# Performance work log

Measured on AMD Instinct MI355X. Metric: run time of the kernel, lower is better.

The kernel has to match this reference:

```python
import jax, jax.numpy as jnp
import numpy as np

H, DH = 8, 64          # num_heads, dim_heads
B, N, D = 1, 4096, 512  # batch, seq, model dim
M, CD = 256, 768        # context len, context dim
J = N + 1 + M           # kv length: self + null + context


def _ln(x, scale, bias, eps=1e-6):
    mu = x.mean(-1, keepdims=True)
    var = ((x - mu) ** 2).mean(-1, keepdims=True)
    return (x - mu) * jax.lax.rsqrt(var + eps) * scale + bias


def setup_inputs() -> dict:
    key = jax.random.key(0)
    ks = jax.random.split(key, 8)
    return {
        'x': jax.random.normal(ks[0], (B, N, D), jnp.float32),
        'context': jax.random.normal(ks[1], (B, M, CD), jnp.float32),
        'attn_bias': jax.random.normal(ks[2], (B, H, N, J), jnp.float32) * 0.02,
        'mask': jnp.ones((B, N + M), dtype=bool),
        'ln1_scale': jnp.ones((D,), jnp.float32),
        'ln1_bias': jnp.zeros((D,), jnp.float32),
        'wq': jax.random.normal(ks[3], (D, H * DH), jnp.float32) * (D ** -0.5),
        'wkv': jax.random.normal(ks[4], (D, 2 * DH), jnp.float32) * (D ** -0.5),
        'null_kv': jax.random.normal(ks[5], (2, DH), jnp.float32),
        'ln_ctx_scale': jnp.ones((CD,), jnp.float32),
        'ln_ctx_bias': jnp.zeros((CD,), jnp.float32),
        'wckv': jax.random.normal(ks[6], (CD, 2 * DH), jnp.float32) * (CD ** -0.5),
        'bckv': jnp.zeros((2 * DH,), jnp.float32),
        'wo': jax.random.normal(ks[7], (H * DH, D), jnp.float32) * ((H * DH) ** -0.5),
        'ln_out_scale': jnp.ones((D,), jnp.float32),
        'ln_out_bias': jnp.zeros((D,), jnp.float32),
    }


def reference(x, context, attn_bias, mask, ln1_scale, ln1_bias, wq, wkv,
              null_kv, ln_ctx_scale, ln_ctx_bias, wckv, bckv, wo,
              ln_out_scale, ln_out_bias):
    b, n, d = x.shape
    scale = DH ** -0.5
    xh = _ln(x, ln1_scale, ln1_bias)
    # multi-query: q has heads, k/v are shared (no head dim)
    q = (xh @ wq).reshape(b, n, H, DH).transpose(0, 2, 1, 3) * scale  # b h n d
    k, v = jnp.split(xh @ wkv, 2, axis=-1)                            # b n d each
    # null kv token appended (per source: concat (k, nk))
    nk = jnp.broadcast_to(null_kv[0], (b, 1, DH))
    nv = jnp.broadcast_to(null_kv[1], (b, 1, DH))
    k = jnp.concatenate((k, nk), axis=-2)
    v = jnp.concatenate((v, nv), axis=-2)
    # cross-attention context kv (Dense with bias)
    ch = _ln(context, ln_ctx_scale, ln_ctx_bias)
    ck, cv = jnp.split(ch @ wckv + bckv, 2, axis=-1)
    k = jnp.concatenate((k, ck), axis=-2)  # b j d, j = n+1+m
    v = jnp.concatenate((v, cv), axis=-2)
    sim = jnp.einsum('bhid,bjd->bhij', q, k) + attn_bias
    # pad mask with True for the extra (null) slot, as in source
    m = jnp.pad(mask, ((0, 0), (1, 0)), constant_values=True)[:, None, None, :]
    sim = jnp.where(m, sim, -jnp.finfo(sim.dtype).max)
    attn = jax.nn.softmax(sim, axis=-1)
    out = jnp.einsum('bhij,bjd->bhid', attn, v)
    out = out.transpose(0, 2, 1, 3).reshape(b, n, H * DH) @ wo
    return _ln(out, ln_out_scale, ln_out_bias)
```

## Files before the change

kernel.cpp:

```cpp
#include <hip/hip_runtime.h>
#include <cstdint>
#include <cstddef>

typedef unsigned short u16;
typedef short s16x8 __attribute__((ext_vector_type(8)));
typedef u16 u16x8 __attribute__((ext_vector_type(8)));
typedef u16 u16x4 __attribute__((ext_vector_type(4)));
typedef float f32x4 __attribute__((ext_vector_type(4)));

#define AS1 __attribute__((address_space(1)))
#define AS3 __attribute__((address_space(3)))

#define HH 8
#define DH 64
#define NN 4096
#define DD 512
#define MM 256
#define CDIM 768
#define JTOT 4353
#define JPAD 4416
#define NJT 69
#define SPLITJ 4
#define TILES_PER_SPLIT 18

static __device__ __forceinline__ u16 f2bf(float f) {
    unsigned int u = __builtin_bit_cast(unsigned int, f);
    u += 0x7FFFu + ((u >> 16) & 1u);
    return (u16)(u >> 16);
}
static __device__ __forceinline__ float bf2f(u16 v) {
    unsigned int u = ((unsigned int)v) << 16;
    return __builtin_bit_cast(float, u);
}

static __device__ __forceinline__ f32x4 mfma16(s16x8 a, s16x8 b, f32x4 c) {
    return __builtin_amdgcn_mfma_f32_16x16x32_bf16(a, b, c, 0, 0, 0);
}

static __device__ __forceinline__ void gload16(const void* g, void* l) {
    __builtin_amdgcn_global_load_lds((const AS1 unsigned int*)g,
                                     (AS3 unsigned int*)l, 16, 0, 0);
}

__global__ void conv_wqkv(const float* __restrict__ wq, const float* __restrict__ wkv,
                          u16* __restrict__ Wt) {
    int idx = blockIdx.x * 256 + threadIdx.x;
    int n = idx >> 9, k = idx & 511;
    float v = (n < 512) ? wq[(size_t)k * 512 + n] * 0.125f
                        : wkv[(size_t)k * 128 + (n - 512)];
    Wt[idx] = f2bf(v);
}

__global__ void conv_wckv(const float* __restrict__ w, u16* __restrict__ Wt) {
    int idx = blockIdx.x * 256 + threadIdx.x;
    int n = idx / 768, k = idx - n * 768;
    Wt[idx] = f2bf(w[(size_t)k * 128 + n]);
}

__global__ void conv_wo(const float* __restrict__ w, u16* __restrict__ Wt) {
    int idx = blockIdx.x * 256 + threadIdx.x;
    int n = idx >> 9, k = idx & 511;
    Wt[idx] = f2bf(w[(size_t)k * 512 + n]);
}

__global__ __launch_bounds__(256) void ln512_to_bf16(
    const float* __restrict__ x, const float* __restrict__ sc,
    const float* __restrict__ bi, u16* __restrict__ out) {
    int row = blockIdx.x * 4 + (threadIdx.x >> 6);
    int lane = threadIdx.x & 63;
    const float4* xp = (const float4*)(x + (size_t)row * 512);
    float4 a = xp[lane], b = xp[64 + lane];
    float s = a.x + a.y + a.z + a.w + b.x + b.y + b.z + b.w;
    float q = a.x*a.x + a.y*a.y + a.z*a.z + a.w*a.w
            + b.x*b.x + b.y*b.y + b.z*b.z + b.w*b.w;
    #pragma unroll
    for (int m = 1; m < 64; m <<= 1) { s += __shfl_xor(s, m); q += __shfl_xor(q, m); }
    float mu = s * (1.f / 512.f);
    float var = q * (1.f / 512.f) - mu * mu;
    float rs = rsqrtf(var + 1e-6f);
    const float4* sp = (const float4*)sc;
    const float4* bp = (const float4*)bi;
    float4 s0 = sp[lane], s1 = sp[64 + lane], b0 = bp[lane], b1 = bp[64 + lane];
    u16x4 o0, o1;
    o0[0] = f2bf((a.x - mu) * rs * s0.x + b0.x);
    o0[1] = f2bf((a.y - mu) * rs * s0.y + b0.y);
    o0[2] = f2bf((a.z - mu) * rs * s0.z + b0.z);
    o0[3] = f2bf((a.w - mu) * rs * s0.w + b0.w);
    o1[0] = f2bf((b.x - mu) * rs * s1.x + b1.x);
    o1[1] = f2bf((b.y - mu) * rs * s1.y + b1.y);
    o1[2] = f2bf((b.z - mu) * rs * s1.z + b1.z);
    o1[3] = f2bf((b.w - mu) * rs * s1.w + b1.w);
    u16x4* op = (u16x4*)(out + (size_t)row * 512);
    op[lane] = o0;
    op[64 + lane] = o1;
}

__global__ __launch_bounds__(256) void ln768_to_bf16(
    const float* __restrict__ x, const float* __restrict__ sc,
    const float* __restrict__ bi, u16* __restrict__ out) {
    int row = blockIdx.x * 4 + (threadIdx.x >> 6);
    int lane = threadIdx.x & 63;
    const float4* xp = (const float4*)(x + (size_t)row * 768);
    float4 a = xp[lane], b = xp[64 + lane], c = xp[128 + lane];
    float s = a.x+a.y+a.z+a.w + b.x+b.y+b.z+b.w + c.x+c.y+c.z+c.w;
    float q = a.x*a.x+a.y*a.y+a.z*a.z+a.w*a.w + b.x*b.x+b.y*b.y+b.z*b.z+b.w*b.w
            + c.x*c.x+c.y*c.y+c.z*c.z+c.w*c.w;
    #pragma unroll
    for (int m = 1; m < 64; m <<= 1) { s += __shfl_xor(s, m); q += __shfl_xor(q, m); }
    float mu = s * (1.f / 768.f);
    float var = q * (1.f / 768.f) - mu * mu;
    float rs = rsqrtf(var + 1e-6f);
    const float4* sp = (const float4*)sc;
    const float4* bp = (const float4*)bi;
    u16x4* op = (u16x4*)(out + (size_t)row * 768);
    #pragma unroll
    for (int seg = 0; seg < 3; ++seg) {
        float4 v = (seg == 0) ? a : (seg == 1) ? b : c;
        float4 ss = sp[seg * 64 + lane], bb = bp[seg * 64 + lane];
        u16x4 o;
        o[0] = f2bf((v.x - mu) * rs * ss.x + bb.x);
        o[1] = f2bf((v.y - mu) * rs * ss.y + bb.y);
        o[2] = f2bf((v.z - mu) * rs * ss.z + bb.z);
        o[3] = f2bf((v.w - mu) * rs * ss.w + bb.w);
        op[seg * 64 + lane] = o;
    }
}

__global__ __launch_bounds__(256) void ln512_to_f32(
    const float* __restrict__ x, const float* __restrict__ sc,
    const float* __restrict__ bi, float* __restrict__ out) {
    int row = blockIdx.x * 4 + (threadIdx.x >> 6);
    int lane = threadIdx.x & 63;
    const float4* xp = (const float4*)(x + (size_t)row * 512);
    float4 a = xp[lane], b = xp[64 + lane];
    float s = a.x + a.y + a.z + a.w + b.x + b.y + b.z + b.w;
    float q = a.x*a.x + a.y*a.y + a.z*a.z + a.w*a.w
            + b.x*b.x + b.y*b.y + b.z*b.z + b.w*b.w;
    #pragma unroll
    for (int m = 1; m < 64; m <<= 1) { s += __shfl_xor(s, m); q += __shfl_xor(q, m); }
    float mu = s * (1.f / 512.f);
    float var = q * (1.f / 512.f) - mu * mu;
    float rs = rsqrtf(var + 1e-6f);
    const float4* sp = (const float4*)sc;
    const float4* bp = (const float4*)bi;
    float4 s0 = sp[lane], s1 = sp[64 + lane], b0 = bp[lane], b1 = bp[64 + lane];
    float4 o0, o1;
    o0.x = (a.x - mu) * rs * s0.x + b0.x;
    o0.y = (a.y - mu) * rs * s0.y + b0.y;
    o0.z = (a.z - mu) * rs * s0.z + b0.z;
    o0.w = (a.w - mu) * rs * s0.w + b0.w;
    o1.x = (b.x - mu) * rs * s1.x + b1.x;
    o1.y = (b.y - mu) * rs * s1.y + b1.y;
    o1.z = (b.z - mu) * rs * s1.z + b1.z;
    o1.w = (b.w - mu) * rs * s1.w + b1.w;
    float4* op = (float4*)(out + (size_t)row * 512);
    op[lane] = o0;
    op[64 + lane] = o1;
}

__global__ void fill_null_pad(const float* __restrict__ null_kv,
                              u16* __restrict__ Kall, u16* __restrict__ Vall) {
    int t = threadIdx.x;
    if (t < 64) {
        Kall[(size_t)4096 * 64 + t] = f2bf(null_kv[t]);
        Vall[(size_t)4096 * 64 + t] = f2bf(null_kv[64 + t]);
    }
    for (int i = t; i < (JPAD - JTOT) * 64; i += 256) {
        Kall[(size_t)JTOT * 64 + i] = 0;
        Vall[(size_t)JTOT * 64 + i] = 0;
    }
}

__global__ __launch_bounds__(256) void gemm_bf16(
    const u16* __restrict__ A, int lda, const u16* __restrict__ Bt, int ldb,
    int M, int N, int K, int mode, const float* __restrict__ bias128,
    u16* __restrict__ outQ, u16* __restrict__ outK, u16* __restrict__ outV,
    float* __restrict__ outF) {
    __shared__ __align__(16) u16 Al[128 * 32];
    __shared__ __align__(16) u16 Bl[64 * 32];
    const int tid = threadIdx.x, wave = tid >> 6, lane = tid & 63;
    const int l16 = lane & 15, l4 = lane >> 4;
    const int m0 = blockIdx.x * 128, n0 = blockIdx.y * 64;

    f32x4 acc[2][4] = {};
    const int ms = tid >> 2, ks = (tid & 3) * 8;

    for (int k0 = 0; k0 < K; k0 += 32) {
        __syncthreads();
        gload16(A + (size_t)(m0 + ms) * lda + (k0 + ks), (char*)Al + wave * 1024);
        gload16(A + (size_t)(m0 + 64 + ms) * lda + (k0 + ks), (char*)Al + 4096 + wave * 1024);
        gload16(Bt + (size_t)(n0 + ms) * ldb + (k0 + ks), (char*)Bl + wave * 1024);
        __syncthreads();
        s16x8 af[2], bf[4];
        #pragma unroll
        for (int mf = 0; mf < 2; ++mf)
            af[mf] = *(const s16x8*)&Al[(wave * 32 + mf * 16 + l16) * 32 + l4 * 8];
        #pragma unroll
        for (int nf = 0; nf < 4; ++nf)
            bf[nf] = *(const s16x8*)&Bl[(nf * 16 + l16) * 32 + l4 * 8];
        #pragma unroll
        for (int mf = 0; mf < 2; ++mf)
            #pragma unroll
            for (int nf = 0; nf < 4; ++nf)
                acc[mf][nf] = mfma16(af[mf], bf[nf], acc[mf][nf]);
    }

    #pragma unroll
    for (int mf = 0; mf < 2; ++mf)
        #pragma unroll
        for (int nf = 0; nf < 4; ++nf)
            #pragma unroll
            for (int r = 0; r < 4; ++r) {
                float v = acc[mf][nf][r];
                int m = m0 + wave * 32 + mf * 16 + l4 * 4 + r;
                int n = n0 + nf * 16 + l16;
                if (mode == 0) {
                    if (n < 512)       outQ[(size_t)m * 512 + n] = f2bf(v);
                    else if (n < 576)  outK[(size_t)m * 64 + (n - 512)] = f2bf(v);
                    else               outV[(size_t)m * 64 + (n - 576)] = f2bf(v);
                } else if (mode == 1) {
                    v += bias128[n];
                    if (n < 64) outK[(size_t)(4097 + m) * 64 + n] = f2bf(v);
                    else        outV[(size_t)(4097 + m) * 64 + (n - 64)] = f2bf(v);
                } else {
                    outF[(size_t)m * 512 + n] = v;
                }
            }
}

__global__ __launch_bounds__(256, 4) void attn_fwd(
    const u16* __restrict__ Q, const u16* __restrict__ Kall,
    const u16* __restrict__ Vall, const float* __restrict__ bias,
    u16* __restrict__ Opart, float* __restrict__ ml) {
    __shared__ __align__(16) u16 Kl[64][72];
    __shared__ __align__(16) u16 Vt[64][72];
    __shared__ __align__(16) u16 Pl[4][16][72];

    const int tid = threadIdx.x, wave = tid >> 6, lane = tid & 63;
    const int l16 = lane & 15, l4 = lane >> 4;
    const int qb = blockIdx.x, h = blockIdx.y, sp = blockIdx.z;
    const int tbeg = sp * TILES_PER_SPLIT;
    const int tend = (tbeg + TILES_PER_SPLIT < NJT) ? tbeg + TILES_PER_SPLIT : NJT;
    const int i0 = qb * 64 + wave * 16;

    const u16* qbase = Q + (size_t)(i0 + l16) * 512 + h * 64 + l4 * 8;
    s16x8 qf0 = *(const s16x8*)qbase;
    s16x8 qf1 = *(const s16x8*)(qbase + 32);

    f32x4 po[4] = {};
    float mrow[4], lrow[4];
    #pragma unroll
    for (int r = 0; r < 4; ++r) { mrow[r] = -3.0e38f; lrow[r] = 0.f; }

    const int krow = tid >> 2, kc = (tid & 3) * 16;
    const int vrow = tid & 63, vd0 = (tid >> 6) * 16;

    const float* brow = bias + ((size_t)h * NN + i0 + l4 * 4) * JTOT;

    u16x8 ks0, ks1, vs0, vs1;
    float bc[16];

#define LOAD_KV(J0) do { \
        const u16* g_ = Kall + (size_t)((J0) + krow) * 64 + kc; \
        ks0 = *(const u16x8*)g_; ks1 = *(const u16x8*)(g_ + 8); \
        const u16* gv_ = Vall + (size_t)((J0) + vrow) * 64 + vd0; \
        vs0 = *(const u16x8*)gv_; vs1 = *(const u16x8*)(gv_ + 8); \
    } while (0)

#define LOAD_BIAS(JT) do { \
        _Pragma("unroll") \
        for (int js_ = 0; js_ < 4; ++js_) { \
            int col_ = (JT) * 64 + js_ * 16 + l16; \
            bool v_ = col_ < JTOT; \
            _Pragma("unroll") \
            for (int r_ = 0; r_ < 4; ++r_) \
                bc[js_ * 4 + r_] = v_ ? brow[(size_t)r_ * JTOT + col_] : 0.f; \
        } \
    } while (0)

#define STORE_LDS() do { \
        *(u16x8*)&Kl[krow][kc]     = ks0; \
        *(u16x8*)&Kl[krow][kc + 8] = ks1; \
        _Pragma("unroll") \
        for (int e_ = 0; e_ < 8; ++e_) Vt[vd0 + e_][vrow] = vs0[e_]; \
        _Pragma("unroll") \
        for (int e_ = 0; e_ < 8; ++e_) Vt[vd0 + 8 + e_][vrow] = vs1[e_]; \
    } while (0)

    LOAD_KV(tbeg * 64);
    LOAD_BIAS(tbeg);
    STORE_LDS();
    __syncthreads();

    for (int jt = tbeg; jt < tend; ++jt) {
        const bool last = (jt == tend - 1);

        f32x4 s[4];
        #pragma unroll
        for (int js = 0; js < 4; ++js) {
            s16x8 kf0 = *(const s16x8*)&Kl[js * 16 + l16][l4 * 8];
            s16x8 kf1 = *(const s16x8*)&Kl[js * 16 + l16][32 + l4 * 8];
            f32x4 z = {};
            z = mfma16(qf0, kf0, z);
            z = mfma16(qf1, kf1, z);
            s[js] = z;
        }
        #pragma unroll
        for (int js = 0; js < 4; ++js) {
            const int col = jt * 64 + js * 16 + l16;
            const bool valid = (col < JTOT);
            #pragma unroll
            for (int r = 0; r < 4; ++r)
                s[js][r] = valid ? s[js][r] + bc[js * 4 + r] : -3.0e38f;
        }
        if (!last) {
            LOAD_BIAS(jt + 1);
            LOAD_KV((jt + 1) * 64);
        }
        float mnew[4], alpha[4];
        #pragma unroll
        for (int r = 0; r < 4; ++r) {
            float t = fmaxf(fmaxf(s[0][r], s[1][r]), fmaxf(s[2][r], s[3][r]));
            t = fmaxf(t, __shfl_xor(t, 1));
            t = fmaxf(t, __shfl_xor(t, 2));
            t = fmaxf(t, __shfl_xor(t, 4));
            t = fmaxf(t, __shfl_xor(t, 8));
            mnew[r] = fmaxf(mrow[r], t);
            alpha[r] = __expf(mrow[r] - mnew[r]);
            mrow[r] = mnew[r];
        }
        #pragma unroll
        for (int js = 0; js < 4; ++js)
            #pragma unroll
            for (int r = 0; r < 4; ++r)
                s[js][r] = __expf(s[js][r] - mnew[r]);
        #pragma unroll
        for (int r = 0; r < 4; ++r) {
            float t = s[0][r] + s[1][r] + s[2][r] + s[3][r];
            t += __shfl_xor(t, 1);
            t += __shfl_xor(t, 2);
            t += __shfl_xor(t, 4);
            t += __shfl_xor(t, 8);
            lrow[r] = lrow[r] * alpha[r] + t;
        }
        #pragma unroll
        for (int df = 0; df < 4; ++df)
            #pragma unroll
            for (int r = 0; r < 4; ++r)
                po[df][r] *= alpha[r];
        #pragma unroll
        for (int js = 0; js < 4; ++js)
            #pragma unroll
            for (int r = 0; r < 4; ++r)
                Pl[wave][l4 * 4 + r][js * 16 + l16] = f2bf(s[js][r]);
        s16x8 pa0 = *(const s16x8*)&Pl[wave][l16][l4 * 8];
        s16x8 pa1 = *(const s16x8*)&Pl[wave][l16][32 + l4 * 8];
        #pragma unroll
        for (int df = 0; df < 4; ++df) {
            s16x8 vf0 = *(const s16x8*)&Vt[df * 16 + l16][l4 * 8];
            s16x8 vf1 = *(const s16x8*)&Vt[df * 16 + l16][32 + l4 * 8];
            po[df] = mfma16(pa0, vf0, po[df]);
            po[df] = mfma16(pa1, vf1, po[df]);
        }
        if (!last) {
            __syncthreads();
            STORE_LDS();
            __syncthreads();
        }
    }

    const size_t obase = (((size_t)sp * 64 + qb) * 8 + h) * 4096;
    #pragma unroll
    for (int df = 0; df < 4; ++df)
        #pragma unroll
        for (int r = 0; r < 4; ++r)
            Opart[obase + (size_t)(wave * 16 + l4 * 4 + r) * 64 + df * 16 + l16] =
                f2bf(po[df][r]);
    const size_t mbase = (((size_t)sp * 64 + qb) * 8 + h) * 128;
    if (l16 == 0) {
        #pragma unroll
        for (int r = 0; r < 4; ++r) {
            ml[mbase + wave * 16 + l4 * 4 + r]      = mrow[r];
            ml[mbase + 64 + wave * 16 + l4 * 4 + r] = lrow[r];
        }
    }
#undef LOAD_KV
#undef LOAD_BIAS
#undef STORE_LDS
}

__global__ __launch_bounds__(256) void attn_combine(
    const u16* __restrict__ Opart, const float* __restrict__ ml,
    u16* __restrict__ Ob) {
    const int qb = blockIdx.x, h = blockIdx.y;
    const int t = threadIdx.x;
    const int row = t >> 2, d0 = (t & 3) * 16;

    float m[SPLITJ], l[SPLITJ];
    #pragma unroll
    for (int s = 0; s < SPLITJ; ++s) {
        const float* mlp = ml + (((size_t)s * 64 + qb) * 8 + h) * 128;
        m[s] = mlp[row];
        l[s] = mlp[64 + row];
    }
    float mstar = m[0];
    #pragma unroll
    for (int s = 1; s < SPLITJ; ++s) mstar = fmaxf(mstar, m[s]);

    float osum[16] = {};
    float lsum = 0.f;
    #pragma unroll
    for (int s = 0; s < SPLITJ; ++s) {
        float w = __expf(m[s] - mstar);
        lsum += w * l[s];
        const u16* op = Opart + ((((size_t)s * 64 + qb) * 8 + h) * 64 + row) * 64 + d0;
        u16x8 a = *(const u16x8*)op;
        u16x8 b = *(const u16x8*)(op + 8);
        #pragma unroll
        for (int e = 0; e < 8; ++e) {
            osum[e]     += w * bf2f(a[e]);
            osum[8 + e] += w * bf2f(b[e]);
        }
    }
    float inv = 1.f / lsum;
    u16x8 oa, obv;
    #pragma unroll
    for (int e = 0; e < 8; ++e) {
        oa[e]  = f2bf(osum[e] * inv);
        obv[e] = f2bf(osum[8 + e] * inv);
    }
    u16* dst = Ob + (size_t)(qb * 64 + row) * 512 + h * 64 + d0;
    *(u16x8*)dst = oa;
    *(u16x8*)(dst + 8) = obv;
}

extern "C" void kernel_launch(void* const* d_in, const int* in_sizes, int n_in,
                              void* d_out, int out_size, void* d_ws, size_t ws_size,
                              hipStream_t stream) {
    (void)in_sizes; (void)n_in; (void)out_size; (void)ws_size;
    const float* x     = (const float*)d_in[0];
    const float* ctx   = (const float*)d_in[1];
    const float* bias  = (const float*)d_in[2];
    const float* ln1s  = (const float*)d_in[4];
    const float* ln1b  = (const float*)d_in[5];
    const float* wq    = (const float*)d_in[6];
    const float* wkv   = (const float*)d_in[7];
    const float* nullkv= (const float*)d_in[8];
    const float* lncs  = (const float*)d_in[9];
    const float* lncb  = (const float*)d_in[10];
    const float* wckv  = (const float*)d_in[11];
    const float* bckv  = (const float*)d_in[12];
    const float* wo    = (const float*)d_in[13];
    const float* lnos  = (const float*)d_in[14];
    const float* lnob  = (const float*)d_in[15];
    float* out = (float*)d_out;

    char* ws = (char*)d_ws;
    u16*   Wo_   = (u16*)(ws + 0);
    u16*   Wqkv  = (u16*)(ws + 524288);
    float* Ml    = (float*)(ws + 524288);
    u16*   Wckv  = (u16*)(ws + 1179648);
    u16*   ch    = (u16*)(ws + 1572864);
    u16*   Qb    = (u16*)(ws + 1966080);
    u16*   Ob    = (u16*)(ws + 1966080);
    u16*   Kall  = (u16*)(ws + 6160384);
    u16*   Vall  = (u16*)(ws + 6725632);
    u16*   xh    = (u16*)(ws + 7290880);
    u16*   Opart = (u16*)(ws + 7290880);
    float* tmp   = (float*)(ws + 7290880);

    conv_wqkv<<<(640 * 512) / 256, 256, 0, stream>>>(wq, wkv, Wqkv);
    conv_wckv<<<(128 * 768) / 256, 256, 0, stream>>>(wckv, Wckv);
    conv_wo<<<(512 * 512) / 256, 256, 0, stream>>>(wo, Wo_);
    ln512_to_bf16<<<1024, 256, 0, stream>>>(x, ln1s, ln1b, xh);
    ln768_to_bf16<<<64, 256, 0, stream>>>(ctx, lncs, lncb, ch);
    fill_null_pad<<<1, 256, 0, stream>>>(nullkv, Kall, Vall);
    gemm_bf16<<<dim3(32, 10), 256, 0, stream>>>(xh, 512, Wqkv, 512, 4096, 640, 512,
                                                0, nullptr, Qb, Kall, Vall, nullptr);
    gemm_bf16<<<dim3(2, 2), 256, 0, stream>>>(ch, 768, Wckv, 768, 256, 128, 768,
                                              1, bckv, nullptr, Kall, Vall, nullptr);
    attn_fwd<<<dim3(64, 8, SPLITJ), 256, 0, stream>>>(Qb, Kall, Vall, bias, Opart, Ml);
    attn_combine<<<dim3(64, 8), 256, 0, stream>>>(Opart, Ml, Ob);
    gemm_bf16<<<dim3(32, 8), 256, 0, stream>>>(Ob, 512, Wo_, 512, 4096, 512, 512,
                                               2, nullptr, nullptr, nullptr, nullptr, tmp);
    ln512_to_f32<<<1024, 256, 0, stream>>>(tmp, lnos, lnob, out);
}
```

Measured before the change: 277.7 us.

## Store V transposed in global memory and read K/V fragments directly, dropping LDS staging

The GEMM epilogues now write V in a transposed [d][JPAD] layout, and the null and pad fill is adjusted to match. The attention kernel loads K and V MFMA fragments straight from global memory (through cache) instead of staging them in LDS with a scattered transpose. This removes two block-wide barriers per tile and the LDS transpose stores. In exchange, each wave issues its own redundant global loads, with no register prefetch ahead of use, so it relies on L1/L2 hits to hide latency. The transposed V stores in the GEMM epilogue are also strided.

```diff
diff --git a/kernel.cpp b/kernel.cpp
--- a/kernel.cpp
+++ b/kernel.cpp
@@ -159,15 +159,16 @@
 }
 
 __global__ void fill_null_pad(const float* __restrict__ null_kv,
-                              u16* __restrict__ Kall, u16* __restrict__ Vall) {
+                              u16* __restrict__ Kall, u16* __restrict__ VallT) {
     int t = threadIdx.x;
     if (t < 64) {
         Kall[(size_t)4096 * 64 + t] = f2bf(null_kv[t]);
-        Vall[(size_t)4096 * 64 + t] = f2bf(null_kv[64 + t]);
+        VallT[(size_t)t * JPAD + 4096] = f2bf(null_kv[64 + t]);
     }
     for (int i = t; i < (JPAD - JTOT) * 64; i += 256) {
         Kall[(size_t)JTOT * 64 + i] = 0;
-        Vall[(size_t)JTOT * 64 + i] = 0;
+        int d = i / (JPAD - JTOT), c = i - d * (JPAD - JTOT);
+        VallT[(size_t)d * JPAD + JTOT + c] = 0;
     }
 }
 
@@ -217,11 +218,11 @@
                 if (mode == 0) {
                     if (n < 512)       outQ[(size_t)m * 512 + n] = f2bf(v);
                     else if (n < 576)  outK[(size_t)m * 64 + (n - 512)] = f2bf(v);
-                    else               outV[(size_t)m * 64 + (n - 576)] = f2bf(v);
+                    else               outV[(size_t)(n - 576) * JPAD + m] = f2bf(v);
                 } else if (mode == 1) {
                     v += bias128[n];
                     if (n < 64) outK[(size_t)(4097 + m) * 64 + n] = f2bf(v);
-                    else        outV[(size_t)(4097 + m) * 64 + (n - 64)] = f2bf(v);
+                    else        outV[(size_t)(n - 64) * JPAD + 4097 + m] = f2bf(v);
                 } else {
                     outF[(size_t)m * 512 + n] = v;
                 }
@@ -230,10 +231,8 @@
 
 __global__ __launch_bounds__(256, 4) void attn_fwd(
     const u16* __restrict__ Q, const u16* __restrict__ Kall,
-    const u16* __restrict__ Vall, const float* __restrict__ bias,
+    const u16* __restrict__ VallT, const float* __restrict__ bias,
     u16* __restrict__ Opart, float* __restrict__ ml) {
-    __shared__ __align__(16) u16 Kl[64][72];
-    __shared__ __align__(16) u16 Vt[64][72];
     __shared__ __align__(16) u16 Pl[4][16][72];
 
     const int tid = threadIdx.x, wave = tid >> 6, lane = tid & 63;
@@ -252,20 +251,11 @@
     #pragma unroll
     for (int r = 0; r < 4; ++r) { mrow[r] = -3.0e38f; lrow[r] = 0.f; }
 
-    const int krow = tid >> 2, kc = (tid & 3) * 16;
-    const int vrow = tid & 63, vd0 = (tid >> 6) * 16;
-
     const float* brow = bias + ((size_t)h * NN + i0 + l4 * 4) * JTOT;
-
-    u16x8 ks0, ks1, vs0, vs1;
+    const u16* kfb = Kall + (size_t)l16 * 64 + l4 * 8;
+    const u16* vfb = VallT + (size_t)l16 * JPAD + l4 * 8;
+
     float bc[16];
-
-#define LOAD_KV(J0) do { \
-        const u16* g_ = Kall + (size_t)((J0) + krow) * 64 + kc; \
-        ks0 = *(const u16x8*)g_; ks1 = *(const u16x8*)(g_ + 8); \
-        const u16* gv_ = Vall + (size_t)((J0) + vrow) * 64 + vd0; \
-        vs0 = *(const u16x8*)gv_; vs1 = *(const u16x8*)(gv_ + 8); \
-    } while (0)
 
 #define LOAD_BIAS(JT) do { \
         _Pragma("unroll") \
@@ -278,28 +268,26 @@
         } \
     } while (0)
 
-#define STORE_LDS() do { \
-        *(u16x8*)&Kl[krow][kc]     = ks0; \
-        *(u16x8*)&Kl[krow][kc + 8] = ks1; \
-        _Pragma("unroll") \
-        for (int e_ = 0; e_ < 8; ++e_) Vt[vd0 + e_][vrow] = vs0[e_]; \
-        _Pragma("unroll") \
-        for (int e_ = 0; e_ < 8; ++e_) Vt[vd0 + 8 + e_][vrow] = vs1[e_]; \
-    } while (0)
-
-    LOAD_KV(tbeg * 64);
     LOAD_BIAS(tbeg);
-    STORE_LDS();
-    __syncthreads();
 
     for (int jt = tbeg; jt < tend; ++jt) {
+        const int j0 = jt * 64;
         const bool last = (jt == tend - 1);
 
+        s16x8 vf0[4], vf1[4];
+        #pragma unroll
+        for (int df = 0; df < 4; ++df) {
+            const u16* p = vfb + (size_t)df * 16 * JPAD + j0;
+            vf0[df] = *(const s16x8*)p;
+            vf1[df] = *(const s16x8*)(p + 32);
+        }
+
         f32x4 s[4];
         #pragma unroll
         for (int js = 0; js < 4; ++js) {
-            s16x8 kf0 = *(const s16x8*)&Kl[js * 16 + l16][l4 * 8];
-            s16x8 kf1 = *(const s16x8*)&Kl[js * 16 + l16][32 + l4 * 8];
+            const u16* kp = kfb + (size_t)(j0 + js * 16) * 64;
+            s16x8 kf0 = *(const s16x8*)kp;
+            s16x8 kf1 = *(const s16x8*)(kp + 32);
             f32x4 z = {};
             z = mfma16(qf0, kf0, z);
             z = mfma16(qf1, kf1, z);
@@ -307,16 +295,14 @@
         }
         #pragma unroll
         for (int js = 0; js < 4; ++js) {
-            const int col = jt * 64 + js * 16 + l16;
+            const int col = j0 + js * 16 + l16;
             const bool valid = (col < JTOT);
             #pragma unroll
             for (int r = 0; r < 4; ++r)
                 s[js][r] = valid ? s[js][r] + bc[js * 4 + r] : -3.0e38f;
         }
-        if (!last) {
-            LOAD_BIAS(jt + 1);
-            LOAD_KV((jt + 1) * 64);
-        }
+        if (!last) LOAD_BIAS(jt + 1);
+
         float mnew[4], alpha[4];
         #pragma unroll
         for (int r = 0; r < 4; ++r) {
@@ -357,15 +343,8 @@
         s16x8 pa1 = *(const s16x8*)&Pl[wave][l16][32 + l4 * 8];
         #pragma unroll
         for (int df = 0; df < 4; ++df) {
-            s16x8 vf0 = *(const s16x8*)&Vt[df * 16 + l16][l4 * 8];
-            s16x8 vf1 = *(const s16x8*)&Vt[df * 16 + l16][32 + l4 * 8];
-            po[df] = mfma16(pa0, vf0, po[df]);
-            po[df] = mfma16(pa1, vf1, po[df]);
-        }
-        if (!last) {
-            __syncthreads();
-            STORE_LDS();
-            __syncthreads();
+            po[df] = mfma16(pa0, vf0[df], po[df]);
+            po[df] = mfma16(pa1, vf1[df], po[df]);
         }
     }
 
@@ -384,9 +363,7 @@
             ml[mbase + 64 + wave * 16 + l4 * 4 + r] = lrow[r];
         }
     }
-#undef LOAD_KV
 #undef LOAD_BIAS
-#undef STORE_LDS
 }
 
 __global__ __launch_bounds__(256) void attn_combine(
@@ -464,7 +441,7 @@
     u16*   Qb    = (u16*)(ws + 1966080);
     u16*   Ob    = (u16*)(ws + 1966080);
     u16*   Kall  = (u16*)(ws + 6160384);
-    u16*   Vall  = (u16*)(ws + 6725632);
+    u16*   VallT = (u16*)(ws + 6725632);
     u16*   xh    = (u16*)(ws + 7290880);
     u16*   Opart = (u16*)(ws + 7290880);
     float* tmp   = (float*)(ws + 7290880);
@@ -474,12 +451,12 @@
     conv_wo<<<(512 * 512) / 256, 256, 0, stream>>>(wo, Wo_);
     ln512_to_bf16<<<1024, 256, 0, stream>>>(x, ln1s, ln1b, xh);
     ln768_to_bf16<<<64, 256, 0, stream>>>(ctx, lncs, lncb, ch);
-    fill_null_pad<<<1, 256, 0, stream>>>(nullkv, Kall, Vall);
+    fill_null_pad<<<1, 256, 0, stream>>>(nullkv, Kall, VallT);
     gemm_bf16<<<dim3(32, 10), 256, 0, stream>>>(xh, 512, Wqkv, 512, 4096, 640, 512,
-                                                0, nullptr, Qb, Kall, Vall, nullptr);
+                                                0, nullptr, Qb, Kall, VallT, nullptr);
     gemm_bf16<<<dim3(2, 2), 256, 0, stream>>>(ch, 768, Wckv, 768, 256, 128, 768,
-                                              1, bckv, nullptr, Kall, Vall, nullptr);
-    attn_fwd<<<dim3(64, 8, SPLITJ), 256, 0, stream>>>(Qb, Kall, Vall, bias, Opart, Ml);
+                                              1, bckv, nullptr, Kall, VallT, nullptr);
+    attn_fwd<<<dim3(64, 8, SPLITJ), 256, 0, stream>>>(Qb, Kall, VallT, bias, Opart, Ml);
     attn_combine<<<dim3(64, 8), 256, 0, stream>>>(Opart, Ml, Ob);
     gemm_bf16<<<dim3(32, 8), 256, 0, stream>>>(Ob, 512, Wo_, 512, 4096, 512, 512,
                                                2, nullptr, nullptr, nullptr, nullptr, tmp);
```

Measured after the change: 447.0 us. +60.9%, slower.
